# Kernel tuning notes

Hardware: AMD Instinct MI355X
Metric: run time of the kernel (lower is better)

## Reference

```python
import jax, jax.numpy as jnp
import numpy as np

B, S, R, H = 32, 512, 49, 768


def setup_inputs() -> dict:
    key = jax.random.key(0)
    ks = jax.random.split(key, 32)
    rn = lambda i, shape, s=1.0: jax.random.normal(ks[i], shape, dtype=jnp.float32) * s
    W = 0.05  # weight init scale to keep tanh/softmax in a sane range
    return {
        'text_features': rn(0, (B, S, H)),
        'img_features': rn(1, (B, R, H)),
        't1_w': rn(2, (H, H), W), 't1_b': rn(3, (H,), W),
        'i1_w': rn(4, (H, H), W),
        'a1_w': rn(5, (2 * H,), W), 'a1_b': rn(6, (), W),
        't2_w': rn(7, (H, H), W),
        'i2_w': rn(8, (H, H), W), 'i2_b': rn(9, (H,), W),
        'a2_w': rn(10, (2 * H,), W), 'a2_b': rn(11, (), W),
        'gt_w': rn(12, (H, H), W), 'gt_b': rn(13, (H,), W),
        'gi_w': rn(14, (H, H), W), 'gi_b': rn(15, (H,), W),
        'gg_w': rn(16, (2 * H, 1), W), 'gg_b': rn(17, (1,), W),
        'ft_w': rn(18, (H, H), W),
        'fm_w': rn(19, (H, H), W), 'fm_b': rn(20, (H,), W),
        'fg_w': rn(21, (2 * H, 1), W), 'fg_b': rn(22, (1,), W),
        'fr_w': rn(23, (H, H), W), 'fr_b': rn(24, (H,), W),
    }


def reference(text_features, img_features, t1_w, t1_b, i1_w, a1_w, a1_b,
              t2_w, i2_w, i2_b, a2_w, a2_b, gt_w, gt_b, gi_w, gi_b,
              gg_w, gg_b, ft_w, fm_w, fm_b, fg_w, fg_b, fr_w, fr_b):
    H = text_features.shape[-1]
    # --- CoAttention, stage 1 (text attends over image regions) ---
    # tanh(concat) is elementwise and att_linear_1 is rank-1, so split the score:
    # score[b,s,r] = tanh(t1(x_s)) . a1[:H] + tanh(i1(y_r)) . a1[H:] + b
    t_sc = jnp.tanh(text_features @ t1_w + t1_b) @ a1_w[:H]          # (B,S)
    i_sc = jnp.tanh(img_features @ i1_w) @ a1_w[H:]                  # (B,R)
    visual_att = jax.nn.softmax(t_sc[:, :, None] + i_sc[:, None, :] + a1_b, axis=-1)  # (B,S,R)
    att_img = jnp.einsum('bsr,brh->bsh', visual_att, img_features)   # (B,S,H)
    # --- CoAttention, stage 2 (attended-image queries attend over text) ---
    # concat order is [img, text] -> a2[:H] pairs with img part
    q_sc = jnp.tanh(att_img @ i2_w + i2_b) @ a2_w[:H]                # (B,S)
    k_sc = jnp.tanh(text_features @ t2_w) @ a2_w[H:]                 # (B,S)
    textual_att = jax.nn.softmax(q_sc[:, :, None] + k_sc[:, None, :] + a2_b, axis=-1)  # (B,S,S)
    att_text = jnp.einsum('bij,bjh->bih', textual_att, text_features)  # (B,S,H)
    # --- GMF gated fusion ---
    new_img = jnp.tanh(att_img @ gi_w + gi_b)
    new_txt = jnp.tanh(att_text @ gt_w + gt_b)
    gate = jax.nn.sigmoid(jnp.concatenate([new_img, new_txt], axis=-1) @ gg_w + gg_b)  # (B,S,1)
    multimodal = gate * new_img + (1.0 - gate) * new_txt
    # --- filtration gate ---
    concat_feat = jnp.concatenate([text_features @ ft_w, multimodal @ fm_w + fm_b], axis=-1)
    fgate = jax.nn.sigmoid(concat_feat @ fg_w + fg_b)                # (B,S,1)
    return fgate * jnp.tanh(multimodal @ fr_w + fr_b)
```

## Files before the change

kernel.cpp:

```cpp
#include <hip/hip_runtime.h>
#include <hip/hip_bf16.h>
#include <math.h>

constexpr int BD = 32;
constexpr int SD = 512;
constexpr int RD = 49;
constexpr int HD = 768;
constexpr int MT = BD * SD;
constexpr int MI = BD * RD;
constexpr int NP = 12;
constexpr int MBT = MT / 128;
constexpr int MBI = 13;
constexpr int NWG = (MBT + MBI) * 6;
constexpr int NT = HD / 32;

typedef __bf16 bf16;
typedef __bf16 bf16x4 __attribute__((ext_vector_type(4)));
typedef __bf16 bf16x8 __attribute__((ext_vector_type(8)));
typedef float f32x4 __attribute__((ext_vector_type(4)));

#define GLOAD_LDS16(g, l) __builtin_amdgcn_global_load_lds( \
    (__attribute__((address_space(1))) void*)(g),           \
    (__attribute__((address_space(3))) void*)(l), 16, 0, 0)
#define BAR() __builtin_amdgcn_s_barrier()
#define SCHED_FENCE() __builtin_amdgcn_sched_barrier(0)
#define WAITV(n) asm volatile("s_waitcnt vmcnt(" #n ")" ::: "memory")

__device__ __forceinline__ float fast_tanh(float x) {
    const float e = __expf(2.f * x);
    return 1.f - 2.f / (e + 1.f);
}

__global__ __launch_bounds__(256) void prep_text(
    const float* __restrict__ text, const float* __restrict__ v_f,
    bf16* __restrict__ text_bf, float* __restrict__ s_txt)
{
    const int row = blockIdx.x * 4 + (threadIdx.x >> 6);
    const int lane = threadIdx.x & 63;
    const float* tr = text + (size_t)row * HD;
    bf16* tb = text_bf + (size_t)row * HD;
    float acc = 0.f;
    #pragma unroll
    for (int c = 0; c < 3; ++c) {
        const int o = c * 256 + lane * 4;
        const f32x4 x = *(const f32x4*)(tr + o);
        const f32x4 v = *(const f32x4*)(v_f + o);
        bf16x4 b; b[0] = (bf16)x[0]; b[1] = (bf16)x[1]; b[2] = (bf16)x[2]; b[3] = (bf16)x[3];
        *(bf16x4*)(tb + o) = b;
        acc += x[0] * v[0] + x[1] * v[1] + x[2] * v[2] + x[3] * v[3];
    }
    for (int off = 32; off; off >>= 1) acc += __shfl_xor(acc, off);
    if (lane == 0) s_txt[row] = acc;
}

__global__ __launch_bounds__(256) void prep_misc(
    const float* __restrict__ ft_w, const float* __restrict__ fm_w,
    const float* __restrict__ fm_b, const float* __restrict__ fg_w,
    float* __restrict__ v_f, float* __restrict__ v_m, float* __restrict__ c_m,
    const float* __restrict__ img, bf16* __restrict__ img_bf,
    const float* __restrict__ t2_w, const float* __restrict__ i1_w,
    bf16* __restrict__ wt_t, bf16* __restrict__ wt_i)
{
    __shared__ float tile[64][65];
    const int bid = blockIdx.x;
    if (bid < 385) {
        const int idx = bid * 4 + (threadIdx.x >> 6);
        const int lane = threadIdx.x & 63;
        const float* row; const float* vecp; float* outp;
        if (idx < HD)            { row = ft_w + (size_t)idx * HD;        vecp = fg_w;      outp = v_f + idx; }
        else if (idx < 2 * HD)   { row = fm_w + (size_t)(idx - HD) * HD; vecp = fg_w + HD; outp = v_m + (idx - HD); }
        else if (idx == 2 * HD)  { row = fm_b;                           vecp = fg_w + HD; outp = c_m; }
        else return;
        float acc = 0.f;
        #pragma unroll
        for (int i = 0; i < HD / 64; ++i) acc += row[lane + 64 * i] * vecp[lane + 64 * i];
        for (int off = 32; off; off >>= 1) acc += __shfl_xor(acc, off);
        if (lane == 0) *outp = acc;
    } else if (bid < 385 + 588) {
        const int i = (bid - 385) * 256 + threadIdx.x;
        const int n8 = BD * RD * HD / 8;
        if (i >= n8) return;
        const size_t o = (size_t)i * 8;
        const f32x4 x0 = *(const f32x4*)(img + o);
        const f32x4 x1 = *(const f32x4*)(img + o + 4);
        bf16x8 b;
        b[0]=(bf16)x0[0]; b[1]=(bf16)x0[1]; b[2]=(bf16)x0[2]; b[3]=(bf16)x0[3];
        b[4]=(bf16)x1[0]; b[5]=(bf16)x1[1]; b[6]=(bf16)x1[2]; b[7]=(bf16)x1[3];
        *(bf16x8*)(img_bf + o) = b;
    } else {
        const int idx2 = bid - (385 + 588);
        const int z = idx2 / 144, rem = idx2 % 144;
        const int bx = rem % 12, by = rem / 12;
        const float* W = z ? i1_w : t2_w;
        bf16* Wt = z ? wt_i : wt_t;
        const int k0 = bx * 64, n0 = by * 64;
        const int t = threadIdx.x;
        const int rb = t >> 6, c = t & 63;
        #pragma unroll
        for (int i = 0; i < 16; ++i) {
            const int r = rb + i * 4;
            tile[r][c] = W[(size_t)(k0 + r) * HD + n0 + c];
        }
        __syncthreads();
        #pragma unroll
        for (int i = 0; i < 16; ++i) {
            const int r = rb + i * 4;
            Wt[(size_t)(n0 + r) * HD + k0 + c] = (bf16)tile[c][r];
        }
    }
}

__global__ __launch_bounds__(256) void gemm2(
    const bf16* __restrict__ Atext, const bf16* __restrict__ WtT,
    const float* __restrict__ vecT, float* __restrict__ partT,
    const bf16* __restrict__ Aimg, const bf16* __restrict__ WtI,
    const float* __restrict__ vecI, float* __restrict__ partI)
{
    __shared__ __align__(16) bf16 As[3 * 4096];
    __shared__ __align__(16) bf16 Bs[3 * 4096];

    const int bid = blockIdx.x;
    const int q = NWG / 8, r = NWG % 8;
    const int xcd = bid % 8, idx = bid / 8;
    const int o = (xcd < r ? xcd * (q + 1) : r * (q + 1) + (xcd - r) * q) + idx;
    const int mb = o / 6, nb = o % 6;

    const bool isT = mb < MBT;
    const bf16* A    = isT ? Atext : Aimg;
    const bf16* Wt   = isT ? WtT : WtI;
    const float* vec = isT ? vecT : vecI;
    float* part      = isT ? partT : partI;
    const int m0 = (isT ? mb : mb - MBT) * 128;
    const int n0 = nb * 128;

    const int t = threadIdx.x;
    const int w = t >> 6, lane = t & 63;
    const int quad = lane >> 4, l16 = lane & 15;
    const int wm2 = (w >> 1) * 64, wn2 = (w & 1) * 64;

    const bf16* Ag = A  + (size_t)(m0 + w * 32 + l16) * HD + quad * 8;
    const bf16* Bg = Wt + (size_t)(n0 + w * 32 + l16) * HD + quad * 8;

    f32x4 acc[4][4] = {};

#define STAGE(tt, ss) {                                       \
    const int ko = (tt) * 32;                                 \
    bf16* a0 = As + (ss) * 4096 + (2 * w) * 512;              \
    bf16* b0 = Bs + (ss) * 4096 + (2 * w) * 512;              \
    GLOAD_LDS16(Ag + ko, a0);                                 \
    GLOAD_LDS16(Ag + (size_t)16 * HD + ko, a0 + 512);         \
    GLOAD_LDS16(Bg + ko, b0);                                 \
    GLOAD_LDS16(Bg + (size_t)16 * HD + ko, b0 + 512);         \
}

#define COMPUTE(ss) {                                                   \
    const bf16* Asl = As + (ss) * 4096;                                 \
    const bf16* Bsl = Bs + (ss) * 4096;                                 \
    bf16x8 af[4], bg4[4];                                               \
    _Pragma("unroll")                                                   \
    for (int f = 0; f < 4; ++f) {                                       \
        af[f]  = *(const bf16x8*)(Asl + (wm2 / 16 + f) * 512 + lane * 8); \
        bg4[f] = *(const bf16x8*)(Bsl + (wn2 / 16 + f) * 512 + lane * 8); \
    }                                                                   \
    _Pragma("unroll")                                                   \
    for (int fi = 0; fi < 4; ++fi)                                      \
        _Pragma("unroll")                                               \
        for (int fj = 0; fj < 4; ++fj)                                  \
            acc[fi][fj] = __builtin_amdgcn_mfma_f32_16x16x32_bf16(af[fi], bg4[fj], acc[fi][fj], 0, 0, 0); \
}

    STAGE(0, 0);
    STAGE(1, 1);

    for (int tt = 0; tt < NT - 2; ++tt) {
        const int s2 = (tt + 2) % 3;
        STAGE(tt + 2, s2);
        WAITV(8);
        BAR();
        SCHED_FENCE();
        COMPUTE(tt % 3);
        SCHED_FENCE();
        BAR();
    }
    WAITV(4);
    BAR();
    SCHED_FENCE();
    COMPUTE((NT - 2) % 3);
    SCHED_FENCE();
    WAITV(0);
    BAR();
    SCHED_FENCE();
    COMPUTE((NT - 1) % 3);

#undef STAGE
#undef COMPUTE

    float vv[4];
    #pragma unroll
    for (int fj = 0; fj < 4; ++fj) vv[fj] = vec[n0 + wn2 + fj * 16 + l16];

    #pragma unroll
    for (int fi = 0; fi < 4; ++fi) {
        #pragma unroll
        for (int reg = 0; reg < 4; ++reg) {
            float p = 0.f;
            #pragma unroll
            for (int fj = 0; fj < 4; ++fj)
                p += fast_tanh(acc[fi][fj][reg]) * vv[fj];
            p += __shfl_xor(p, 1);
            p += __shfl_xor(p, 2);
            p += __shfl_xor(p, 4);
            p += __shfl_xor(p, 8);
            if (l16 == 0) {
                const int row = m0 + wm2 + fi * 16 + quad * 4 + reg;
                part[(size_t)row * NP + nb * 2 + (w & 1)] = p;
            }
        }
    }
}

__global__ __launch_bounds__(256) void red_soft(
    const float* __restrict__ k_part, const float* __restrict__ i_part,
    float* __restrict__ k_sc, float* __restrict__ i_sc)
{
    __shared__ float red[4];
    if (blockIdx.x < BD) {
        const int b = blockIdx.x, t = threadIdx.x;
        const float* p0 = k_part + ((size_t)b * SD + t) * NP;
        const float* p1 = k_part + ((size_t)b * SD + 256 + t) * NP;
        float x0 = 0.f, x1 = 0.f;
        #pragma unroll
        for (int j = 0; j < 3; ++j) {
            const f32x4 a = *(const f32x4*)(p0 + j * 4);
            const f32x4 c = *(const f32x4*)(p1 + j * 4);
            x0 += a[0] + a[1] + a[2] + a[3];
            x1 += c[0] + c[1] + c[2] + c[3];
        }
        float m = fmaxf(x0, x1);
        for (int off = 32; off; off >>= 1) m = fmaxf(m, __shfl_xor(m, off));
        if ((t & 63) == 0) red[t >> 6] = m;
        __syncthreads();
        m = fmaxf(fmaxf(red[0], red[1]), fmaxf(red[2], red[3]));
        const float e0 = expf(x0 - m), e1 = expf(x1 - m);
        float s = e0 + e1;
        for (int off = 32; off; off >>= 1) s += __shfl_xor(s, off);
        __syncthreads();
        if ((t & 63) == 0) red[t >> 6] = s;
        __syncthreads();
        s = red[0] + red[1] + red[2] + red[3];
        k_sc[b * SD + t] = e0 / s;
        k_sc[b * SD + 256 + t] = e1 / s;
    } else {
        const int b = blockIdx.x - BD, l = threadIdx.x;
        if (l < 64) {
            float x = -1e30f;
            if (l < RD) {
                const float* p = i_part + ((size_t)(b * RD + l)) * NP;
                float s0 = 0.f;
                #pragma unroll
                for (int j = 0; j < 3; ++j) {
                    const f32x4 a = *(const f32x4*)(p + j * 4);
                    s0 += a[0] + a[1] + a[2] + a[3];
                }
                x = s0;
            }
            float m = x;
            for (int off = 32; off; off >>= 1) m = fmaxf(m, __shfl_xor(m, off));
            float e = (l < RD) ? expf(x - m) : 0.f;
            float s = e;
            for (int off = 32; off; off >>= 1) s += __shfl_xor(s, off);
            if (l < RD) i_sc[b * RD + l] = e / s;
        }
    }
}

__global__ __launch_bounds__(256) void wsum_both(
    const float* __restrict__ P1, const float* __restrict__ img,
    float* __restrict__ aimg,
    const float* __restrict__ P2, const bf16* __restrict__ text_bf,
    float* __restrict__ ws_part)
{
    __shared__ float Ps[SD];
    const int bid = blockIdx.x;
    if (bid < 96) {
        const int b = bid & 31, hy = bid >> 5;
        const int h = hy * 256 + threadIdx.x;
        for (int j = threadIdx.x; j < RD; j += 256) Ps[j] = P1[b * RD + j];
        __syncthreads();
        float acc = 0.f;
        const float* Xb = img + (size_t)b * RD * HD + h;
        for (int j = 0; j < RD; ++j) acc += Ps[j] * Xb[(size_t)j * HD];
        aimg[b * HD + h] = acc;
    } else {
        const int idx = bid - 96;
        const int q = idx / 96, rem = idx % 96;
        const int b = rem & 31, hy = rem >> 5;
        const int h = hy * 256 + threadIdx.x;
        if (threadIdx.x < 128) Ps[threadIdx.x] = P2[b * SD + q * 128 + threadIdx.x];
        __syncthreads();
        float acc = 0.f;
        const bf16* Xb = text_bf + (size_t)b * SD * HD + (size_t)(q * 128) * HD + h;
        #pragma unroll 8
        for (int j = 0; j < 128; ++j) acc += Ps[j] * (float)Xb[(size_t)j * HD];
        ws_part[((size_t)(b * 4 + q)) * HD + h] = acc;
    }
}

__global__ __launch_bounds__(256) void ni_nt_kernel(
    const float* __restrict__ aimg, const float* __restrict__ ws_part,
    const float* __restrict__ gi_w, const float* __restrict__ gi_b,
    const float* __restrict__ gt_w, const float* __restrict__ gt_b,
    float* __restrict__ ni, float* __restrict__ nt)
{
    const int b = blockIdx.x, n0 = blockIdx.y * 64, which = blockIdx.z;
    const float* W = which ? gt_w : gi_w;
    const float* bias = which ? gt_b : gi_b;
    float* Y = which ? nt : ni;

    __shared__ float Xs[HD];
    __shared__ float partial[4][64];
    const int t = threadIdx.x;
    if (which) {
        for (int h = t; h < HD; h += 256)
            Xs[h] = ws_part[((size_t)(b * 4 + 0)) * HD + h] + ws_part[((size_t)(b * 4 + 1)) * HD + h]
                  + ws_part[((size_t)(b * 4 + 2)) * HD + h] + ws_part[((size_t)(b * 4 + 3)) * HD + h];
    } else {
        for (int h = t; h < HD; h += 256) Xs[h] = aimg[b * HD + h];
    }
    __syncthreads();
    const int n = n0 + (t & 63), kq = t >> 6;
    float acc = 0.f;
    const float* Wp = W + (size_t)(kq * 192) * HD + n;
    #pragma unroll 8
    for (int h = 0; h < 192; ++h) acc += Xs[kq * 192 + h] * Wp[(size_t)h * HD];
    partial[kq][t & 63] = acc;
    __syncthreads();
    if (t < 64) {
        const float s = partial[0][t] + partial[1][t] + partial[2][t] + partial[3][t];
        Y[b * HD + n0 + t] = tanhf(s + bias[n0 + t]);
    }
}

__global__ __launch_bounds__(256) void gate_mix(
    const float* __restrict__ ni, const float* __restrict__ nt,
    const float* __restrict__ gg_w, const float* __restrict__ gg_b,
    const float* __restrict__ v_m, const float* __restrict__ c_m,
    const float* __restrict__ fg_b,
    float* __restrict__ mm, float* __restrict__ s_mm)
{
    const int b = blockIdx.x, t = threadIdx.x;
    __shared__ float red[4];
    __shared__ float gsh;
    float acc = 0.f;
    for (int n = t; n < HD; n += 256)
        acc += ni[b * HD + n] * gg_w[n] + nt[b * HD + n] * gg_w[HD + n];
    for (int off = 32; off; off >>= 1) acc += __shfl_xor(acc, off);
    if ((t & 63) == 0) red[t >> 6] = acc;
    __syncthreads();
    if (t == 0) gsh = 1.f / (1.f + expf(-(red[0] + red[1] + red[2] + red[3] + gg_b[0])));
    __syncthreads();
    const float g = gsh;
    float a2 = 0.f;
    for (int n = t; n < HD; n += 256) {
        const float m = g * ni[b * HD + n] + (1.f - g) * nt[b * HD + n];
        mm[b * HD + n] = m;
        a2 += m * v_m[n];
    }
    for (int off = 32; off; off >>= 1) a2 += __shfl_xor(a2, off);
    __syncthreads();
    if ((t & 63) == 0) red[t >> 6] = a2;
    __syncthreads();
    if (t == 0) s_mm[b] = red[0] + red[1] + red[2] + red[3] + *c_m + fg_b[0];
}

__global__ __launch_bounds__(256) void T_kernel(
    const float* __restrict__ mm, const float* __restrict__ fr_w,
    const float* __restrict__ fr_b, float* __restrict__ T)
{
    const int b = blockIdx.x, n0 = blockIdx.y * 64;
    __shared__ float Xs[HD];
    __shared__ float partial[4][64];
    const int t = threadIdx.x;
    for (int h = t; h < HD; h += 256) Xs[h] = mm[b * HD + h];
    __syncthreads();
    const int n = n0 + (t & 63), kq = t >> 6;
    float acc = 0.f;
    const float* Wp = fr_w + (size_t)(kq * 192) * HD + n;
    #pragma unroll 8
    for (int h = 0; h < 192; ++h) acc += Xs[kq * 192 + h] * Wp[(size_t)h * HD];
    partial[kq][t & 63] = acc;
    __syncthreads();
    if (t < 64) {
        const float s = partial[0][t] + partial[1][t] + partial[2][t] + partial[3][t];
        T[b * HD + n0 + t] = tanhf(s + fr_b[n0 + t]);
    }
}

__global__ __launch_bounds__(256) void out_kernel(const float* __restrict__ s_txt,
                                                  const float* __restrict__ s_mm,
                                                  const float* __restrict__ T,
                                                  float* __restrict__ out) {
    const size_t idx = ((size_t)blockIdx.x * 256 + threadIdx.x) * 4;
    const int h = (int)(idx % HD);
    const int bs = (int)(idx / HD);
    const int b = bs >> 9;
    float f = s_txt[bs] + s_mm[b];
    f = 1.f / (1.f + expf(-f));
    const float* Tp = T + b * HD + h;
    f32x4 o;
    o[0] = f * Tp[0]; o[1] = f * Tp[1]; o[2] = f * Tp[2]; o[3] = f * Tp[3];
    *(f32x4*)(out + idx) = o;
}

extern "C" void kernel_launch(void* const* d_in, const int* in_sizes, int n_in,
                              void* d_out, int out_size, void* d_ws, size_t ws_size,
                              hipStream_t stream) {
    const float* text = (const float*)d_in[0];
    const float* img  = (const float*)d_in[1];
    const float* i1_w = (const float*)d_in[4];
    const float* a1_w = (const float*)d_in[5];
    const float* t2_w = (const float*)d_in[7];
    const float* a2_w = (const float*)d_in[10];
    const float* gt_w = (const float*)d_in[12];
    const float* gt_b = (const float*)d_in[13];
    const float* gi_w = (const float*)d_in[14];
    const float* gi_b = (const float*)d_in[15];
    const float* gg_w = (const float*)d_in[16];
    const float* gg_b = (const float*)d_in[17];
    const float* ft_w = (const float*)d_in[18];
    const float* fm_w = (const float*)d_in[19];
    const float* fm_b = (const float*)d_in[20];
    const float* fg_w = (const float*)d_in[21];
    const float* fg_b = (const float*)d_in[22];
    const float* fr_w = (const float*)d_in[23];
    const float* fr_b = (const float*)d_in[24];
    float* out = (float*)d_out;

    float* sc_ = out;
    float* i_part  = sc_;
    float* k_part  = sc_ + 38400;
    float* i_sc    = sc_ + 431616;
    float* k_sc    = sc_ + 433216;
    float* aimg    = sc_ + 449600;
    float* v_f     = sc_ + 498752;
    float* v_m     = sc_ + 499520;
    float* c_m     = sc_ + 500288;
    float* ws_part = sc_ + 500352;
    float* ni      = sc_ + 598656;
    float* nt      = sc_ + 623232;
    float* mm      = sc_ + 647808;
    bf16* text_bf  = (bf16*)(sc_ + 672384);
    bf16* img_bf   = (bf16*)(sc_ + 6963840);
    bf16* wt_t     = (bf16*)(sc_ + 7565952);
    bf16* wt_i     = (bf16*)(sc_ + 7860864);

    float* ws    = (float*)d_ws;
    float* s_txt = ws;
    float* s_mm  = ws + 16384;
    float* T     = ws + 16448;

    prep_misc<<<dim3(385 + 588 + 288), dim3(256), 0, stream>>>(
        ft_w, fm_w, fm_b, fg_w, v_f, v_m, c_m, img, img_bf, t2_w, i1_w, wt_t, wt_i);
    prep_text<<<dim3(MT / 4), dim3(256), 0, stream>>>(text, v_f, text_bf, s_txt);
    gemm2<<<dim3(NWG), dim3(256), 0, stream>>>(
        text_bf, wt_t, a2_w + HD, k_part, img_bf, wt_i, a1_w + HD, i_part);
    red_soft<<<dim3(2 * BD), dim3(256), 0, stream>>>(k_part, i_part, k_sc, i_sc);
    wsum_both<<<dim3(96 + 384), dim3(256), 0, stream>>>(
        i_sc, img, aimg, k_sc, text_bf, ws_part);
    ni_nt_kernel<<<dim3(BD, HD / 64, 2), dim3(256), 0, stream>>>(
        aimg, ws_part, gi_w, gi_b, gt_w, gt_b, ni, nt);
    gate_mix<<<dim3(BD), dim3(256), 0, stream>>>(
        ni, nt, gg_w, gg_b, v_m, c_m, fg_b, mm, s_mm);
    T_kernel<<<dim3(BD, HD / 64), dim3(256), 0, stream>>>(mm, fr_w, fr_b, T);
    out_kernel<<<dim3((MT * HD / 4) / 256), dim3(256), 0, stream>>>(s_txt, s_mm, T, out);
}
```

Before: 275.1 us.

## Simplify gemm2 pipeline to single-buffer BK=64 and fuse gate_mix into T kernel

The projection GEMM drops its three-stage global-to-LDS pipeline with explicit waitcnt and barriers. It now loads a 64-wide K slice into one buffer, syncs, computes two MFMA sub-steps, and syncs again, with a launch bound allowing four workgroups per CU. This cuts LDS use so more workgroups can share a CU and hide latency, but it gives up the overlap between loads and compute inside a workgroup. Separately, gate_mix and T_kernel are fused into one gateT kernel that recomputes the gate and mix per block in shared memory, removing one launch and the round trip through the mm buffer at the cost of redundant gate computation.

```diff
diff --git a/kernel.cpp b/kernel.cpp
--- a/kernel.cpp
+++ b/kernel.cpp
@@ -12,7 +12,7 @@
 constexpr int MBT = MT / 128;
 constexpr int MBI = 13;
 constexpr int NWG = (MBT + MBI) * 6;
-constexpr int NT = HD / 32;
+constexpr int NT2 = HD / 64;
 
 typedef __bf16 bf16;
 typedef __bf16 bf16x4 __attribute__((ext_vector_type(4)));
@@ -22,9 +22,6 @@
 #define GLOAD_LDS16(g, l) __builtin_amdgcn_global_load_lds( \
     (__attribute__((address_space(1))) void*)(g),           \
     (__attribute__((address_space(3))) void*)(l), 16, 0, 0)
-#define BAR() __builtin_amdgcn_s_barrier()
-#define SCHED_FENCE() __builtin_amdgcn_sched_barrier(0)
-#define WAITV(n) asm volatile("s_waitcnt vmcnt(" #n ")" ::: "memory")
 
 __device__ __forceinline__ float fast_tanh(float x) {
     const float e = __expf(2.f * x);
@@ -110,19 +107,19 @@
     }
 }
 
-__global__ __launch_bounds__(256) void gemm2(
+__global__ __launch_bounds__(256, 4) void gemm2(
     const bf16* __restrict__ Atext, const bf16* __restrict__ WtT,
     const float* __restrict__ vecT, float* __restrict__ partT,
     const bf16* __restrict__ Aimg, const bf16* __restrict__ WtI,
     const float* __restrict__ vecI, float* __restrict__ partI)
 {
-    __shared__ __align__(16) bf16 As[3 * 4096];
-    __shared__ __align__(16) bf16 Bs[3 * 4096];
+    __shared__ __align__(16) bf16 As[16 * 512];
+    __shared__ __align__(16) bf16 Bs[16 * 512];
 
     const int bid = blockIdx.x;
     const int q = NWG / 8, r = NWG % 8;
-    const int xcd = bid % 8, idx = bid / 8;
-    const int o = (xcd < r ? xcd * (q + 1) : r * (q + 1) + (xcd - r) * q) + idx;
+    const int xcd = bid % 8, sidx = bid / 8;
+    const int o = (xcd < r ? xcd * (q + 1) : r * (q + 1) + (xcd - r) * q) + sidx;
     const int mb = o / 6, nb = o % 6;
 
     const bool isT = mb < MBT;
@@ -138,62 +135,40 @@
     const int quad = lane >> 4, l16 = lane & 15;
     const int wm2 = (w >> 1) * 64, wn2 = (w & 1) * 64;
 
-    const bf16* Ag = A  + (size_t)(m0 + w * 32 + l16) * HD + quad * 8;
-    const bf16* Bg = Wt + (size_t)(n0 + w * 32 + l16) * HD + quad * 8;
+    const bf16* Ag = A  + (size_t)(m0 + l16) * HD + quad * 8;
+    const bf16* Bg = Wt + (size_t)(n0 + l16) * HD + quad * 8;
 
     f32x4 acc[4][4] = {};
 
-#define STAGE(tt, ss) {                                       \
-    const int ko = (tt) * 32;                                 \
-    bf16* a0 = As + (ss) * 4096 + (2 * w) * 512;              \
-    bf16* b0 = Bs + (ss) * 4096 + (2 * w) * 512;              \
-    GLOAD_LDS16(Ag + ko, a0);                                 \
-    GLOAD_LDS16(Ag + (size_t)16 * HD + ko, a0 + 512);         \
-    GLOAD_LDS16(Bg + ko, b0);                                 \
-    GLOAD_LDS16(Bg + (size_t)16 * HD + ko, b0 + 512);         \
-}
-
-#define COMPUTE(ss) {                                                   \
-    const bf16* Asl = As + (ss) * 4096;                                 \
-    const bf16* Bsl = Bs + (ss) * 4096;                                 \
-    bf16x8 af[4], bg4[4];                                               \
-    _Pragma("unroll")                                                   \
-    for (int f = 0; f < 4; ++f) {                                       \
-        af[f]  = *(const bf16x8*)(Asl + (wm2 / 16 + f) * 512 + lane * 8); \
-        bg4[f] = *(const bf16x8*)(Bsl + (wn2 / 16 + f) * 512 + lane * 8); \
-    }                                                                   \
-    _Pragma("unroll")                                                   \
-    for (int fi = 0; fi < 4; ++fi)                                      \
-        _Pragma("unroll")                                               \
-        for (int fj = 0; fj < 4; ++fj)                                  \
-            acc[fi][fj] = __builtin_amdgcn_mfma_f32_16x16x32_bf16(af[fi], bg4[fj], acc[fi][fj], 0, 0, 0); \
-}
-
-    STAGE(0, 0);
-    STAGE(1, 1);
-
-    for (int tt = 0; tt < NT - 2; ++tt) {
-        const int s2 = (tt + 2) % 3;
-        STAGE(tt + 2, s2);
-        WAITV(8);
-        BAR();
-        SCHED_FENCE();
-        COMPUTE(tt % 3);
-        SCHED_FENCE();
-        BAR();
-    }
-    WAITV(4);
-    BAR();
-    SCHED_FENCE();
-    COMPUTE((NT - 2) % 3);
-    SCHED_FENCE();
-    WAITV(0);
-    BAR();
-    SCHED_FENCE();
-    COMPUTE((NT - 1) % 3);
-
-#undef STAGE
-#undef COMPUTE
+    for (int tt = 0; tt < NT2; ++tt) {
+        const int kk = tt * 64;
+        #pragma unroll
+        for (int h = 0; h < 2; ++h) {
+            #pragma unroll
+            for (int j = 0; j < 2; ++j) {
+                const int rc = 2 * w + j;
+                GLOAD_LDS16(Ag + (size_t)rc * 16 * HD + kk + h * 32, As + (h * 8 + rc) * 512);
+                GLOAD_LDS16(Bg + (size_t)rc * 16 * HD + kk + h * 32, Bs + (h * 8 + rc) * 512);
+            }
+        }
+        __syncthreads();
+
+        #pragma unroll
+        for (int h = 0; h < 2; ++h) {
+            bf16x8 af[4], bg4[4];
+            #pragma unroll
+            for (int f = 0; f < 4; ++f) {
+                af[f]  = *(const bf16x8*)(As + (h * 8 + wm2 / 16 + f) * 512 + lane * 8);
+                bg4[f] = *(const bf16x8*)(Bs + (h * 8 + wn2 / 16 + f) * 512 + lane * 8);
+            }
+            #pragma unroll
+            for (int fi = 0; fi < 4; ++fi)
+                #pragma unroll
+                for (int fj = 0; fj < 4; ++fj)
+                    acc[fi][fj] = __builtin_amdgcn_mfma_f32_16x16x32_bf16(af[fi], bg4[fj], acc[fi][fj], 0, 0, 0);
+        }
+        __syncthreads();
+    }
 
     float vv[4];
     #pragma unroll
@@ -341,19 +316,26 @@
     }
 }
 
-__global__ __launch_bounds__(256) void gate_mix(
+__global__ __launch_bounds__(256) void gateT(
     const float* __restrict__ ni, const float* __restrict__ nt,
     const float* __restrict__ gg_w, const float* __restrict__ gg_b,
     const float* __restrict__ v_m, const float* __restrict__ c_m,
     const float* __restrict__ fg_b,
-    float* __restrict__ mm, float* __restrict__ s_mm)
-{
-    const int b = blockIdx.x, t = threadIdx.x;
+    const float* __restrict__ fr_w, const float* __restrict__ fr_b,
+    float* __restrict__ T, float* __restrict__ s_mm)
+{
+    const int b = blockIdx.x, n0 = blockIdx.y * 64, t = threadIdx.x;
+    __shared__ float Ni[HD], Nt[HD], Mm[HD];
+    __shared__ float partial[4][64];
     __shared__ float red[4];
     __shared__ float gsh;
+
     float acc = 0.f;
-    for (int n = t; n < HD; n += 256)
-        acc += ni[b * HD + n] * gg_w[n] + nt[b * HD + n] * gg_w[HD + n];
+    for (int n = t; n < HD; n += 256) {
+        const float vi = ni[b * HD + n], vt = nt[b * HD + n];
+        Ni[n] = vi; Nt[n] = vt;
+        acc += vi * gg_w[n] + vt * gg_w[HD + n];
+    }
     for (int off = 32; off; off >>= 1) acc += __shfl_xor(acc, off);
     if ((t & 63) == 0) red[t >> 6] = acc;
     __syncthreads();
@@ -362,33 +344,26 @@
     const float g = gsh;
     float a2 = 0.f;
     for (int n = t; n < HD; n += 256) {
-        const float m = g * ni[b * HD + n] + (1.f - g) * nt[b * HD + n];
-        mm[b * HD + n] = m;
+        const float m = g * Ni[n] + (1.f - g) * Nt[n];
+        Mm[n] = m;
         a2 += m * v_m[n];
     }
-    for (int off = 32; off; off >>= 1) a2 += __shfl_xor(a2, off);
-    __syncthreads();
-    if ((t & 63) == 0) red[t >> 6] = a2;
-    __syncthreads();
-    if (t == 0) s_mm[b] = red[0] + red[1] + red[2] + red[3] + *c_m + fg_b[0];
-}
-
-__global__ __launch_bounds__(256) void T_kernel(
-    const float* __restrict__ mm, const float* __restrict__ fr_w,
-    const float* __restrict__ fr_b, float* __restrict__ T)
-{
-    const int b = blockIdx.x, n0 = blockIdx.y * 64;
-    __shared__ float Xs[HD];
-    __shared__ float partial[4][64];
-    const int t = threadIdx.x;
-    for (int h = t; h < HD; h += 256) Xs[h] = mm[b * HD + h];
     __syncthreads();
     const int n = n0 + (t & 63), kq = t >> 6;
-    float acc = 0.f;
+    float tacc = 0.f;
     const float* Wp = fr_w + (size_t)(kq * 192) * HD + n;
     #pragma unroll 8
-    for (int h = 0; h < 192; ++h) acc += Xs[kq * 192 + h] * Wp[(size_t)h * HD];
-    partial[kq][t & 63] = acc;
+    for (int h = 0; h < 192; ++h) tacc += Mm[kq * 192 + h] * Wp[(size_t)h * HD];
+    partial[kq][t & 63] = tacc;
+    if (blockIdx.y == 0) {
+        for (int off = 32; off; off >>= 1) a2 += __shfl_xor(a2, off);
+        __syncthreads();
+        if ((t & 63) == 0) red[t >> 6] = a2;
+        __syncthreads();
+        if (t == 0) s_mm[b] = red[0] + red[1] + red[2] + red[3] + *c_m + fg_b[0];
+    } else {
+        __syncthreads();
+    }
     __syncthreads();
     if (t < 64) {
         const float s = partial[0][t] + partial[1][t] + partial[2][t] + partial[3][t];
@@ -448,7 +423,6 @@
     float* ws_part = sc_ + 500352;
     float* ni      = sc_ + 598656;
     float* nt      = sc_ + 623232;
-    float* mm      = sc_ + 647808;
     bf16* text_bf  = (bf16*)(sc_ + 672384);
     bf16* img_bf   = (bf16*)(sc_ + 6963840);
     bf16* wt_t     = (bf16*)(sc_ + 7565952);
@@ -469,8 +443,7 @@
         i_sc, img, aimg, k_sc, text_bf, ws_part);
     ni_nt_kernel<<<dim3(BD, HD / 64, 2), dim3(256), 0, stream>>>(
         aimg, ws_part, gi_w, gi_b, gt_w, gt_b, ni, nt);
-    gate_mix<<<dim3(BD), dim3(256), 0, stream>>>(
-        ni, nt, gg_w, gg_b, v_m, c_m, fg_b, mm, s_mm);
-    T_kernel<<<dim3(BD, HD / 64), dim3(256), 0, stream>>>(mm, fr_w, fr_b, T);
+    gateT<<<dim3(BD, HD / 64), dim3(256), 0, stream>>>(
+        ni, nt, gg_w, gg_b, v_m, c_m, fg_b, fr_w, fr_b, T, s_mm);
     out_kernel<<<dim3((MT * HD / 4) / 256), dim3(256), 0, stream>>>(s_txt, s_mm, T, out);
 }
```

Result: faster. 266.5 us (-3.1%).
